# Optimization experiments

Measured on AMD Instinct MI355X. Metric: run time of the kernel, lower is better.

## Reference

```python
import jax, jax.numpy as jnp
import numpy as np

NHEAD = 8
GROUPS = 32   # GroupNorm(32) assumed for ConvNormActivation's norm (diffusion-UNet convention)
EPS = 1e-5


def group_norm(x, scale, bias):
    # x: [B, C, H, W]
    b, c, h, w = x.shape
    xg = x.reshape(b, GROUPS, c // GROUPS, h, w)
    mu = xg.mean(axis=(2, 3, 4), keepdims=True)
    var = xg.var(axis=(2, 3, 4), keepdims=True)
    xg = (xg - mu) * jax.lax.rsqrt(var + EPS)
    return xg.reshape(b, c, h, w) * scale[None, :, None, None] + bias[None, :, None, None]


def setup_inputs() -> dict:
    key = jax.random.key(0)
    ks = jax.random.split(key, 3)
    B, C, H, W = 8, 512, 32, 32
    s = 0.02
    return {
        "x": jax.random.normal(ks[0], (B, C, H, W), jnp.float32),
        "gn1_scale": jnp.ones((C,), jnp.float32),
        "gn1_bias": jnp.zeros((C,), jnp.float32),
        "w_qkv": jax.random.normal(ks[1], (3 * C, C), jnp.float32) * s,  # 1x1 conv kernel
        "b_qkv": jnp.zeros((3 * C,), jnp.float32),
        "w_proj": jax.random.normal(ks[2], (C, C), jnp.float32) * s,    # 1x1 conv kernel
        "b_proj": jnp.zeros((C,), jnp.float32),
        "gn2_scale": jnp.ones((C,), jnp.float32),
        "gn2_bias": jnp.zeros((C,), jnp.float32),
    }


def reference(x, gn1_scale, gn1_bias, w_qkv, b_qkv, w_proj, b_proj, gn2_scale, gn2_bias):
    b, c, h, w = x.shape
    n = h * w
    ch = c // NHEAD

    # qkv = Conv1x1(GroupNorm(x))  (norm_first=True)
    hn = group_norm(x, gn1_scale, gn1_bias)
    qkv = jnp.einsum('bchw,oc->bohw', hn, w_qkv) + b_qkv[None, :, None, None]

    # [B, 3C, H, W] -> [B*heads, 3*ch, N], split into q,k,v (matches torch reshape/split)
    qkv = qkv.reshape(b * NHEAD, 3 * ch, n)
    q, k, v = jnp.split(qkv, 3, axis=1)

    scale = ch ** -0.25
    wgt = jnp.einsum('bct,bcs->bts', q * scale, k * scale)   # [B*H, N, N]
    wgt = jax.nn.softmax(wgt, axis=-1)                        # stable (max-subtract fused)
    a = jnp.einsum('bts,bcs->bct', wgt, v).reshape(b, c, h, w)

    # proj_out = GroupNorm(Conv1x1(a))  (norm after conv, Identity activation)
    out = jnp.einsum('bchw,oc->bohw', a, w_proj) + b_proj[None, :, None, None]
    out = group_norm(out, gn2_scale, gn2_bias)
    return x + out
```

## Files before the change

kernel.cpp:

```cpp
#include <hip/hip_runtime.h>
#include <math.h>

#define NB 8
#define NC 512
#define NHW 1024
#define NG 32
#define CPG 16
#define QKV_C 1536
#define EPS 1e-5f
#define QSCALE 0.18033688011112042f

typedef float  f32x4  __attribute__((ext_vector_type(4)));
typedef __bf16 bf16x8 __attribute__((ext_vector_type(8)));
typedef __bf16 bf16x4 __attribute__((ext_vector_type(4)));
typedef short  s16x4  __attribute__((ext_vector_type(4)));

__device__ __forceinline__ void gload_lds16(const void* g, void* l) {
    __builtin_amdgcn_global_load_lds(
        (const __attribute__((address_space(1))) void*)g,
        (__attribute__((address_space(3))) void*)l, 16, 0, 0);
}

__device__ __forceinline__ void dma_drain() {
    asm volatile("s_waitcnt vmcnt(0)" ::: "memory");
}

__device__ __forceinline__ f32x4 mfma16(bf16x4 a, bf16x4 b, f32x4 c) {
#if __has_builtin(__builtin_amdgcn_mfma_f32_16x16x16bf16_1k)
    return __builtin_amdgcn_mfma_f32_16x16x16bf16_1k(
        __builtin_bit_cast(s16x4, a), __builtin_bit_cast(s16x4, b), c, 0, 0, 0);
#else
    f32x4 d;
    asm volatile("v_mfma_f32_16x16x16_bf16 %0, %1, %2, %3"
                 : "=v"(d) : "v"(a), "v"(b), "v"(c));
    return d;
#endif
}

__global__ __launch_bounds__(256) void prep_k(const float* __restrict__ x,
                                              float* __restrict__ mu,
                                              float* __restrict__ rinv,
                                              const float* __restrict__ w1,
                                              __bf16* __restrict__ d1,
                                              const float* __restrict__ w2,
                                              __bf16* __restrict__ d2,
                                              float* __restrict__ gstat) {
    const int bi = blockIdx.x;
    if (bi < 256) {
        const int grp = bi;
        const float4* p4 = (const float4*)(x + (size_t)grp * (CPG * NHW));
        float s = 0.f, s2 = 0.f;
        for (int i = threadIdx.x; i < CPG * NHW / 4; i += 256) {
            float4 v = p4[i];
            s  += v.x + v.y + v.z + v.w;
            s2 += v.x * v.x + v.y * v.y + v.z * v.z + v.w * v.w;
        }
        for (int off = 32; off > 0; off >>= 1) {
            s  += __shfl_down(s, off);
            s2 += __shfl_down(s2, off);
        }
        __shared__ float ls[4], ls2[4];
        const int wv = threadIdx.x >> 6;
        if ((threadIdx.x & 63) == 0) { ls[wv] = s; ls2[wv] = s2; }
        __syncthreads();
        if (threadIdx.x == 0) {
            float S = ls[0] + ls[1] + ls[2] + ls[3];
            float S2 = ls2[0] + ls2[1] + ls2[2] + ls2[3];
            const float inv = 1.f / (float)(CPG * NHW);
            float m = S * inv;
            float var = S2 * inv - m * m;
            mu[grp] = m;
            rinv[grp] = rsqrtf(var + EPS);
        }
        if (bi == 0 && threadIdx.x < 256) {
            gstat[threadIdx.x] = 0.f;
            gstat[threadIdx.x + 256] = 0.f;
        }
    } else {
        const int n1_4 = QKV_C * NC / 4;
        const int i = (bi - 256) * 256 + threadIdx.x;
        const float4* s = (i < n1_4) ? (const float4*)w1 + i
                                     : (const float4*)w2 + (i - n1_4);
        bf16x4* d = (i < n1_4) ? (bf16x4*)d1 + i : (bf16x4*)d2 + (i - n1_4);
        float4 v = *s;
        bf16x4 o;
        o[0] = (__bf16)v.x; o[1] = (__bf16)v.y; o[2] = (__bf16)v.z; o[3] = (__bf16)v.w;
        *d = o;
    }
}

__global__ __launch_bounds__(256) void gn_apply_t_k(const float* __restrict__ x,
                                                    const float* __restrict__ mu,
                                                    const float* __restrict__ rinv,
                                                    const float* __restrict__ sc,
                                                    const float* __restrict__ bi,
                                                    __bf16* __restrict__ hnT) {
    __shared__ float T[64][65];
    const int tid = threadIdx.x;
    const int nb = blockIdx.x * 64, cb = blockIdx.y * 64, b = blockIdx.z;
    const int col = (tid & 15) * 4;
    const int rb = tid >> 4;
    #pragma unroll
    for (int rr = 0; rr < 4; rr++) {
        int cl = rr * 16 + rb;
        int c = cb + cl;
        int grp = b * NG + (c >> 4);
        float a = sc[c] * rinv[grp];
        float d = bi[c] - mu[grp] * a;
        float4 v4 = *(const float4*)&x[((size_t)(b * NC + c)) * NHW + nb + col];
        T[cl][col + 0] = v4.x * a + d;
        T[cl][col + 1] = v4.y * a + d;
        T[cl][col + 2] = v4.z * a + d;
        T[cl][col + 3] = v4.w * a + d;
    }
    __syncthreads();
    const int nl = tid >> 2;
    const int c0 = (tid & 3) * 16;
    bf16x8 o0, o1;
    #pragma unroll
    for (int i = 0; i < 8; i++) o0[i] = (__bf16)T[c0 + i][nl];
    #pragma unroll
    for (int i = 0; i < 8; i++) o1[i] = (__bf16)T[c0 + 8 + i][nl];
    __bf16* dst = hnT + ((size_t)(b * NHW + nb + nl)) * NC + cb + c0;
    *(bf16x8*)dst = o0;
    *(bf16x8*)(dst + 8) = o1;
}

__device__ __forceinline__ void mm_stage(const __bf16* __restrict__ W,
                                         const __bf16* __restrict__ Bm,
                                         int K, int m0, int n0, int k0,
                                         __bf16* As, __bf16* Bs) {
    const int tid = threadIdx.x;
    const int w = tid >> 6, lane = tid & 63;
    const int lr = lane >> 2, lk = (lane & 3) * 8;
    #pragma unroll
    for (int i = 0; i < 2; i++) {
        int rb = (w * 2 + i) * 16;
        gload_lds16(W  + (size_t)(m0 + rb + lr) * K + k0 + lk, As + rb * 32);
        gload_lds16(Bm + (size_t)(n0 + rb + lr) * K + k0 + lk, Bs + rb * 32);
    }
}

__device__ __forceinline__ void mm_core(const __bf16* __restrict__ W,
                                        const __bf16* __restrict__ Bm,
                                        int K, int m0, int n0,
                                        __bf16* As, __bf16* Bs,
                                        f32x4 (&acc)[4][4]) {
    const int tid = threadIdx.x;
    const int w = tid >> 6, lane = tid & 63;
    const int l15 = lane & 15, quad = lane >> 4;
    const int wm = (w & 1) * 64, wn = (w >> 1) * 64;
    const int nk = K >> 5;
    mm_stage(W, Bm, K, m0, n0, 0, As, Bs);
    for (int it = 0; it < nk; it++) {
        const int cur = (it & 1) * 4096;
        dma_drain();
        __syncthreads();
        if (it + 1 < nk)
            mm_stage(W, Bm, K, m0, n0, (it + 1) * 32, As + (4096 - cur), Bs + (4096 - cur));
        bf16x8 af[4], bfv[4];
        #pragma unroll
        for (int mi = 0; mi < 4; mi++)
            af[mi] = *(const bf16x8*)(As + cur + (wm + mi * 16 + l15) * 32 + quad * 8);
        #pragma unroll
        for (int ni = 0; ni < 4; ni++)
            bfv[ni] = *(const bf16x8*)(Bs + cur + (wn + ni * 16 + l15) * 32 + quad * 8);
        #pragma unroll
        for (int mi = 0; mi < 4; mi++)
            #pragma unroll
            for (int ni = 0; ni < 4; ni++)
                acc[mi][ni] = __builtin_amdgcn_mfma_f32_16x16x32_bf16(
                    af[mi], bfv[ni], acc[mi][ni], 0, 0, 0);
    }
}

__global__ __launch_bounds__(256) void qkv_gemm_k(const __bf16* __restrict__ W,
                                                  const __bf16* __restrict__ hnT,
                                                  const float* __restrict__ bias,
                                                  __bf16* __restrict__ qT,
                                                  __bf16* __restrict__ kT,
                                                  __bf16* __restrict__ v) {
    __shared__ __bf16 As[2 * 128 * 32];
    __shared__ __bf16 Bs[2 * 128 * 32];
    const int m0 = blockIdx.x * 128, n0 = blockIdx.y * 128, b = blockIdx.z;
    f32x4 acc[4][4] = {};
    mm_core(W, hnT + (size_t)b * NHW * NC, NC, m0, n0, As, Bs, acc);
    const int tid = threadIdx.x;
    const int w = tid >> 6, lane = tid & 63;
    const int l15 = lane & 15, quad = lane >> 4;
    const int wm = (w & 1) * 64, wn = (w >> 1) * 64;
    #pragma unroll
    for (int mi = 0; mi < 4; mi++) {
        #pragma unroll
        for (int r = 0; r < 4; r++) {
            int m = m0 + wm + mi * 16 + quad * 4 + r;
            float bb = bias[m];
            int h = m / 192;
            int rr = m - h * 192;
            int bh = b * 8 + h;
            #pragma unroll
            for (int ni = 0; ni < 4; ni++) {
                int n = n0 + wn + ni * 16 + l15;
                float val = acc[mi][ni][r] + bb;
                if (rr < 64) {
                    qT[((size_t)bh << 16) + n * 64 + rr] = (__bf16)(val * QSCALE);
                } else if (rr < 128) {
                    kT[((size_t)bh << 16) + n * 64 + (rr - 64)] = (__bf16)val;
                } else {
                    v[((size_t)(bh * 64 + rr - 128)) * NHW + n] = (__bf16)val;
                }
            }
        }
    }
}

__global__ __launch_bounds__(256) void proj_gemm_k(const __bf16* __restrict__ W,
                                                   const __bf16* __restrict__ aT,
                                                   const float* __restrict__ bias,
                                                   __bf16* __restrict__ projb,
                                                   float* __restrict__ gstat) {
    __shared__ __bf16 As[2 * 128 * 32];
    __shared__ __bf16 Bs[2 * 128 * 32];
    const int m0 = blockIdx.x * 128, n0 = blockIdx.y * 128, b = blockIdx.z;
    f32x4 acc[4][4] = {};
    mm_core(W, aT + (size_t)b * NHW * NC, NC, m0, n0, As, Bs, acc);
    const int tid = threadIdx.x;
    const int w = tid >> 6, lane = tid & 63;
    const int l15 = lane & 15, quad = lane >> 4;
    const int wm = (w & 1) * 64, wn = (w >> 1) * 64;
    float bsum[4] = {}, bsq[4] = {};
    #pragma unroll
    for (int mi = 0; mi < 4; mi++) {
        #pragma unroll
        for (int r = 0; r < 4; r++) {
            int m = m0 + wm + mi * 16 + quad * 4 + r;
            float bb = bias[m];
            #pragma unroll
            for (int ni = 0; ni < 4; ni++) {
                int n = n0 + wn + ni * 16 + l15;
                float val = acc[mi][ni][r] + bb;
                projb[((size_t)(b * NC + m)) * NHW + n] = (__bf16)val;
                bsum[mi] += val;
                bsq[mi] += val * val;
            }
        }
    }
    #pragma unroll
    for (int mi = 0; mi < 4; mi++) {
        float s = bsum[mi], q = bsq[mi];
        #pragma unroll
        for (int off = 1; off < 64; off <<= 1) {
            s += __shfl_xor(s, off);
            q += __shfl_xor(q, off);
        }
        if (lane == 0) {
            int grp = b * NG + ((m0 + wm) >> 4) + mi;
            atomicAdd(&gstat[grp], s);
            atomicAdd(&gstat[256 + grp], q);
        }
    }
}

__global__ __launch_bounds__(256) void attn_k(const __bf16* __restrict__ qT,
                                              const __bf16* __restrict__ kT,
                                              const __bf16* __restrict__ vv,
                                              __bf16* __restrict__ aT) {
    __shared__ __bf16 Kt[2 * 4096];
    __shared__ __bf16 Vt[2 * 4096];
    const int tid = threadIdx.x;
    const int w = tid >> 6, lane = tid & 63;
    const int l15 = lane & 15, quad = lane >> 4;
    const int lr = lane >> 2, lk = (lane & 3) * 8;
    const int bh = blockIdx.x, t0 = blockIdx.y * 128;
    const __bf16* qb = qT + ((size_t)bh << 16);
    const __bf16* kb = kT + ((size_t)bh << 16);
    const __bf16* vb = vv + ((size_t)bh << 6) * NHW;
    const int xmask = l15 & 14;

    bf16x8 qfr[2][2];
    #pragma unroll
    for (int tb = 0; tb < 2; tb++)
        #pragma unroll
        for (int ch = 0; ch < 2; ch++)
            qfr[tb][ch] = *(const bf16x8*)(qb + (size_t)(t0 + w * 32 + tb * 16 + l15) * 64
                                           + ch * 32 + quad * 8);
    #pragma unroll
    for (int i = 0; i < 4; i++) {
        int inst = w * 4 + i;
        if (inst < 8) {
            int ch = inst >> 2, sb = (inst & 3) * 16;
            gload_lds16(kb + (size_t)(sb + lr) * 64 + ch * 32 + lk,
                        Kt + ch * 2048 + sb * 32);
        } else {
            int ip = inst - 8;
            int c = ip * 8 + (lane >> 3);
            int m2 = (lane & 7) * 2;
            gload_lds16(vb + (size_t)c * NHW + 4 * (m2 ^ (c & 14)),
                        Vt + ip * 512);
        }
    }
    float lp[2] = {0.f, 0.f};
    f32x4 Oacc[2][4] = {};

    for (int it = 0; it < 16; it++) {
        const int cur = (it & 1) * 4096;
        const int nxt = 4096 - cur;
        dma_drain();
        __syncthreads();
        if (it + 1 < 16) {
            const int s0 = (it + 1) * 64;
            #pragma unroll
            for (int i = 0; i < 4; i++) {
                int inst = w * 4 + i;
                if (inst < 8) {
                    int ch = inst >> 2, sb = (inst & 3) * 16;
                    gload_lds16(kb + (size_t)(s0 + sb + lr) * 64 + ch * 32 + lk,
                                Kt + nxt + ch * 2048 + sb * 32);
                } else {
                    int ip = inst - 8;
                    int c = ip * 8 + (lane >> 3);
                    int m2 = (lane & 7) * 2;
                    gload_lds16(vb + (size_t)c * NHW + s0 + 4 * (m2 ^ (c & 14)),
                                Vt + nxt + ip * 512);
                }
            }
        }
        f32x4 sacc[2][4] = {};
        #pragma unroll
        for (int ch = 0; ch < 2; ch++)
            #pragma unroll
            for (int j = 0; j < 4; j++) {
                bf16x8 kfr = *(const bf16x8*)(Kt + cur + ch * 2048
                                              + (j * 16 + l15) * 32 + quad * 8);
                sacc[0][j] = __builtin_amdgcn_mfma_f32_16x16x32_bf16(
                    kfr, qfr[0][ch], sacc[0][j], 0, 0, 0);
                sacc[1][j] = __builtin_amdgcn_mfma_f32_16x16x32_bf16(
                    kfr, qfr[1][ch], sacc[1][j], 0, 0, 0);
            }
        bf16x4 pf[2][4];
        #pragma unroll
        for (int tb = 0; tb < 2; tb++)
            #pragma unroll
            for (int j = 0; j < 4; j++) {
                bf16x4 pk;
                #pragma unroll
                for (int r = 0; r < 4; r++) {
                    float pv = __builtin_amdgcn_exp2f(sacc[tb][j][r]);
                    lp[tb] += pv;
                    pk[r] = (__bf16)pv;
                }
                pf[tb][j] = pk;
            }
        #pragma unroll
        for (int jt = 0; jt < 4; jt++) {
            const __bf16* vbase = Vt + cur + (((jt * 4 + quad) ^ xmask) << 2);
            #pragma unroll
            for (int ci = 0; ci < 4; ci++) {
                bf16x4 vfr = *(const bf16x4*)(vbase + (ci * 16 + l15) * 64);
                Oacc[0][ci] = mfma16(pf[0][jt], vfr, Oacc[0][ci]);
                Oacc[1][ci] = mfma16(pf[1][jt], vfr, Oacc[1][ci]);
            }
        }
    }
    const int b = bh >> 3, hh = bh & 7;
    #pragma unroll
    for (int tb = 0; tb < 2; tb++) {
        float s = lp[tb];
        s += __shfl_xor(s, 16);
        s += __shfl_xor(s, 32);
        #pragma unroll
        for (int r = 0; r < 4; r++) {
            float inv = 1.f / __shfl(s, quad * 4 + r);
            int t = t0 + w * 32 + tb * 16 + quad * 4 + r;
            size_t base = ((size_t)(b * NHW + t)) * NC + hh * 64;
            #pragma unroll
            for (int ci = 0; ci < 4; ci++)
                aT[base + ci * 16 + l15] = (__bf16)(Oacc[tb][ci][r] * inv);
        }
    }
}

__global__ __launch_bounds__(256) void final_k(const float* __restrict__ x,
                                               const __bf16* __restrict__ pb,
                                               const float* __restrict__ gstat,
                                               const float* __restrict__ sc,
                                               const float* __restrict__ bi,
                                               float* __restrict__ out) {
    const int i4 = blockIdx.x * 256 + threadIdx.x;
    const int c  = (i4 >> 8) & (NC - 1);
    const int b  = i4 >> 17;
    const int grp = b * NG + (c >> 4);
    const float inv = 1.f / (float)(CPG * NHW);
    const float m = gstat[grp] * inv;
    const float var = gstat[256 + grp] * inv - m * m;
    const float r = rsqrtf(var + EPS);
    const float a = sc[c] * r;
    const float d = bi[c] - m * a;
    float4 xv = ((const float4*)x)[i4];
    bf16x4 pv = ((const bf16x4*)pb)[i4];
    float4 o = make_float4(xv.x + (float)pv[0] * a + d, xv.y + (float)pv[1] * a + d,
                           xv.z + (float)pv[2] * a + d, xv.w + (float)pv[3] * a + d);
    ((float4*)out)[i4] = o;
}

extern "C" void kernel_launch(void* const* d_in, const int* in_sizes, int n_in,
                              void* d_out, int out_size, void* d_ws, size_t ws_size,
                              hipStream_t stream) {
    const float* x      = (const float*)d_in[0];
    const float* gn1_s  = (const float*)d_in[1];
    const float* gn1_b  = (const float*)d_in[2];
    const float* w_qkv  = (const float*)d_in[3];
    const float* b_qkv  = (const float*)d_in[4];
    const float* w_proj = (const float*)d_in[5];
    const float* b_proj = (const float*)d_in[6];
    const float* gn2_s  = (const float*)d_in[7];
    const float* gn2_b  = (const float*)d_in[8];
    float* out = (float*)d_out;

    char* p = (char*)d_ws;
    __bf16* hnT   = (__bf16*)p;           p += (size_t)8 * 1024 * 512 * 2;
    __bf16* qT    = (__bf16*)p;           p += (size_t)64 * 1024 * 64 * 2;
    __bf16* kT    = (__bf16*)p;           p += (size_t)64 * 1024 * 64 * 2;
    __bf16* vB    = (__bf16*)p;           p += (size_t)64 * 64 * 1024 * 2;
    __bf16* aT    = (__bf16*)p;           p += (size_t)8 * 1024 * 512 * 2;
    __bf16* projb = (__bf16*)p;           p += (size_t)8 * 512 * 1024 * 2;
    __bf16* wq    = (__bf16*)p;           p += (size_t)QKV_C * NC * 2;
    __bf16* wp    = (__bf16*)p;           p += (size_t)NC * NC * 2;
    float*  mu1   = (float*)p;            p += 256 * 4;
    float*  ri1   = (float*)p;            p += 256 * 4;
    float*  gstat = (float*)p;            p += 512 * 4;

    prep_k<<<1280, 256, 0, stream>>>(x, mu1, ri1, w_qkv, wq, w_proj, wp, gstat);
    gn_apply_t_k<<<dim3(16, 8, 8), 256, 0, stream>>>(x, mu1, ri1, gn1_s, gn1_b, hnT);

    qkv_gemm_k<<<dim3(12, 8, 8), 256, 0, stream>>>(wq, hnT, b_qkv, qT, kT, vB);

    attn_k<<<dim3(64, 8), 256, 0, stream>>>(qT, kT, vB, aT);

    proj_gemm_k<<<dim3(4, 8, 8), 256, 0, stream>>>(wp, aT, b_proj, projb, gstat);

    final_k<<<4096, 256, 0, stream>>>(x, projb, gstat, gn2_s, gn2_b, out);
}
```

Before: 181.4 us.

## Split attention keys across waves, halve proj tile, vectorize qkv epilogue stores

The attention kernel now processes 64 queries per block, with each wave handling a distinct 16-key slice. Partial outputs and row sums are reduced across waves through shared memory, and the result is written as 16-byte vectors. This doubles the grid to 1024 blocks for better occupancy. The projection GEMM uses 64-row tiles with its own inline loop, doubling its grid, and the QKV epilogue writes q/k as bf16x4 vectors with a vector bias load. The cost is a serialized four-phase cross-wave reduction through shared memory and more K/V reloads per query.

Result: slower. 187.1 us (+3.2%).

```diff
diff --git a/kernel.cpp b/kernel.cpp
--- a/kernel.cpp
+++ b/kernel.cpp
@@ -191,53 +191,95 @@
     const int wm = (w & 1) * 64, wn = (w >> 1) * 64;
     #pragma unroll
     for (int mi = 0; mi < 4; mi++) {
-        #pragma unroll
-        for (int r = 0; r < 4; r++) {
-            int m = m0 + wm + mi * 16 + quad * 4 + r;
-            float bb = bias[m];
-            int h = m / 192;
-            int rr = m - h * 192;
-            int bh = b * 8 + h;
-            #pragma unroll
-            for (int ni = 0; ni < 4; ni++) {
-                int n = n0 + wn + ni * 16 + l15;
-                float val = acc[mi][ni][r] + bb;
-                if (rr < 64) {
-                    qT[((size_t)bh << 16) + n * 64 + rr] = (__bf16)(val * QSCALE);
-                } else if (rr < 128) {
-                    kT[((size_t)bh << 16) + n * 64 + (rr - 64)] = (__bf16)val;
-                } else {
-                    v[((size_t)(bh * 64 + rr - 128)) * NHW + n] = (__bf16)val;
-                }
+        const int mbase = m0 + wm + mi * 16 + quad * 4;
+        const f32x4 bb4 = *(const f32x4*)&bias[mbase];
+        const int h = mbase / 192;
+        const int rr = mbase - h * 192;
+        const int bh = b * 8 + h;
+        #pragma unroll
+        for (int ni = 0; ni < 4; ni++) {
+            const int n = n0 + wn + ni * 16 + l15;
+            f32x4 a4 = acc[mi][ni];
+            if (rr < 64) {
+                bf16x4 o;
+                #pragma unroll
+                for (int r = 0; r < 4; r++) o[r] = (__bf16)((a4[r] + bb4[r]) * QSCALE);
+                *(bf16x4*)&qT[((size_t)bh << 16) + n * 64 + rr] = o;
+            } else if (rr < 128) {
+                bf16x4 o;
+                #pragma unroll
+                for (int r = 0; r < 4; r++) o[r] = (__bf16)(a4[r] + bb4[r]);
+                *(bf16x4*)&kT[((size_t)bh << 16) + n * 64 + (rr - 64)] = o;
+            } else {
+                #pragma unroll
+                for (int r = 0; r < 4; r++)
+                    v[((size_t)(bh * 64 + rr - 128 + r)) * NHW + n] = (__bf16)(a4[r] + bb4[r]);
             }
         }
     }
 }
 
 __global__ __launch_bounds__(256) void proj_gemm_k(const __bf16* __restrict__ W,
-                                                   const __bf16* __restrict__ aT,
+                                                   const __bf16* __restrict__ aTin,
                                                    const float* __restrict__ bias,
                                                    __bf16* __restrict__ projb,
                                                    float* __restrict__ gstat) {
-    __shared__ __bf16 As[2 * 128 * 32];
+    __shared__ __bf16 As[2 * 64 * 32];
     __shared__ __bf16 Bs[2 * 128 * 32];
-    const int m0 = blockIdx.x * 128, n0 = blockIdx.y * 128, b = blockIdx.z;
-    f32x4 acc[4][4] = {};
-    mm_core(W, aT + (size_t)b * NHW * NC, NC, m0, n0, As, Bs, acc);
+    const int m0 = blockIdx.x * 64, n0 = blockIdx.y * 128, b = blockIdx.z;
+    const __bf16* Bm = aTin + (size_t)b * NHW * NC;
     const int tid = threadIdx.x;
     const int w = tid >> 6, lane = tid & 63;
     const int l15 = lane & 15, quad = lane >> 4;
-    const int wm = (w & 1) * 64, wn = (w >> 1) * 64;
+    const int lr = lane >> 2, lk = (lane & 3) * 8;
+    f32x4 acc[4][2] = {};
+    {
+        gload_lds16(W + (size_t)(m0 + w * 16 + lr) * NC + lk, As + (w * 16) * 32);
+        #pragma unroll
+        for (int i = 0; i < 2; i++) {
+            int rb = w * 32 + i * 16;
+            gload_lds16(Bm + (size_t)(n0 + rb + lr) * NC + lk, Bs + rb * 32);
+        }
+    }
+    for (int it = 0; it < 16; it++) {
+        const int curA = (it & 1) * 2048, curB = (it & 1) * 4096;
+        dma_drain();
+        __syncthreads();
+        if (it + 1 < 16) {
+            const int k0 = (it + 1) * 32;
+            gload_lds16(W + (size_t)(m0 + w * 16 + lr) * NC + k0 + lk,
+                        As + (2048 - curA) + (w * 16) * 32);
+            #pragma unroll
+            for (int i = 0; i < 2; i++) {
+                int rb = w * 32 + i * 16;
+                gload_lds16(Bm + (size_t)(n0 + rb + lr) * NC + k0 + lk,
+                            Bs + (4096 - curB) + rb * 32);
+            }
+        }
+        bf16x8 af[4], bfv[2];
+        #pragma unroll
+        for (int mi = 0; mi < 4; mi++)
+            af[mi] = *(const bf16x8*)(As + curA + (mi * 16 + l15) * 32 + quad * 8);
+        #pragma unroll
+        for (int ni = 0; ni < 2; ni++)
+            bfv[ni] = *(const bf16x8*)(Bs + curB + (w * 32 + ni * 16 + l15) * 32 + quad * 8);
+        #pragma unroll
+        for (int mi = 0; mi < 4; mi++)
+            #pragma unroll
+            for (int ni = 0; ni < 2; ni++)
+                acc[mi][ni] = __builtin_amdgcn_mfma_f32_16x16x32_bf16(
+                    af[mi], bfv[ni], acc[mi][ni], 0, 0, 0);
+    }
     float bsum[4] = {}, bsq[4] = {};
     #pragma unroll
     for (int mi = 0; mi < 4; mi++) {
         #pragma unroll
         for (int r = 0; r < 4; r++) {
-            int m = m0 + wm + mi * 16 + quad * 4 + r;
+            int m = m0 + mi * 16 + quad * 4 + r;
             float bb = bias[m];
             #pragma unroll
-            for (int ni = 0; ni < 4; ni++) {
-                int n = n0 + wn + ni * 16 + l15;
+            for (int ni = 0; ni < 2; ni++) {
+                int n = n0 + w * 32 + ni * 16 + l15;
                 float val = acc[mi][ni][r] + bb;
                 projb[((size_t)(b * NC + m)) * NHW + n] = (__bf16)val;
                 bsum[mi] += val;
@@ -254,7 +296,7 @@
             q += __shfl_xor(q, off);
         }
         if (lane == 0) {
-            int grp = b * NG + ((m0 + wm) >> 4) + mi;
+            int grp = b * NG + (m0 >> 4) + mi;
             atomicAdd(&gstat[grp], s);
             atomicAdd(&gstat[256 + grp], q);
         }
@@ -265,24 +307,27 @@
                                               const __bf16* __restrict__ kT,
                                               const __bf16* __restrict__ vv,
                                               __bf16* __restrict__ aT) {
-    __shared__ __bf16 Kt[2 * 4096];
-    __shared__ __bf16 Vt[2 * 4096];
+    __shared__ __align__(16) char smem[32768];
+    __bf16* Kt = (__bf16*)smem;
+    __bf16* Vt = (__bf16*)(smem + 16384);
+    float*  Om = (float*)smem;
+    float*  Lr = (float*)(smem + 17408);
     const int tid = threadIdx.x;
     const int w = tid >> 6, lane = tid & 63;
     const int l15 = lane & 15, quad = lane >> 4;
     const int lr = lane >> 2, lk = (lane & 3) * 8;
-    const int bh = blockIdx.x, t0 = blockIdx.y * 128;
+    const int bh = blockIdx.x, t0 = blockIdx.y * 64;
     const __bf16* qb = qT + ((size_t)bh << 16);
     const __bf16* kb = kT + ((size_t)bh << 16);
     const __bf16* vb = vv + ((size_t)bh << 6) * NHW;
     const int xmask = l15 & 14;
 
-    bf16x8 qfr[2][2];
-    #pragma unroll
-    for (int tb = 0; tb < 2; tb++)
+    bf16x8 qfr[4][2];
+    #pragma unroll
+    for (int tb = 0; tb < 4; tb++)
         #pragma unroll
         for (int ch = 0; ch < 2; ch++)
-            qfr[tb][ch] = *(const bf16x8*)(qb + (size_t)(t0 + w * 32 + tb * 16 + l15) * 64
+            qfr[tb][ch] = *(const bf16x8*)(qb + (size_t)(t0 + tb * 16 + l15) * 64
                                            + ch * 32 + quad * 8);
     #pragma unroll
     for (int i = 0; i < 4; i++) {
@@ -299,8 +344,8 @@
                         Vt + ip * 512);
         }
     }
-    float lp[2] = {0.f, 0.f};
-    f32x4 Oacc[2][4] = {};
+    float lp[4] = {};
+    f32x4 Oacc[4][4] = {};
 
     for (int it = 0; it < 16; it++) {
         const int cur = (it & 1) * 4096;
@@ -325,59 +370,77 @@
                 }
             }
         }
-        f32x4 sacc[2][4] = {};
-        #pragma unroll
-        for (int ch = 0; ch < 2; ch++)
-            #pragma unroll
-            for (int j = 0; j < 4; j++) {
-                bf16x8 kfr = *(const bf16x8*)(Kt + cur + ch * 2048
-                                              + (j * 16 + l15) * 32 + quad * 8);
-                sacc[0][j] = __builtin_amdgcn_mfma_f32_16x16x32_bf16(
-                    kfr, qfr[0][ch], sacc[0][j], 0, 0, 0);
-                sacc[1][j] = __builtin_amdgcn_mfma_f32_16x16x32_bf16(
-                    kfr, qfr[1][ch], sacc[1][j], 0, 0, 0);
+        f32x4 sacc[4] = {};
+        #pragma unroll
+        for (int ch = 0; ch < 2; ch++) {
+            bf16x8 kfr = *(const bf16x8*)(Kt + cur + ch * 2048
+                                          + (w * 16 + l15) * 32 + quad * 8);
+            #pragma unroll
+            for (int tb = 0; tb < 4; tb++)
+                sacc[tb] = __builtin_amdgcn_mfma_f32_16x16x32_bf16(
+                    kfr, qfr[tb][ch], sacc[tb], 0, 0, 0);
+        }
+        bf16x4 pf[4];
+        #pragma unroll
+        for (int tb = 0; tb < 4; tb++) {
+            bf16x4 pk;
+            #pragma unroll
+            for (int r = 0; r < 4; r++) {
+                float pv = __builtin_amdgcn_exp2f(sacc[tb][r]);
+                lp[tb] += pv;
+                pk[r] = (__bf16)pv;
             }
-        bf16x4 pf[2][4];
-        #pragma unroll
-        for (int tb = 0; tb < 2; tb++)
-            #pragma unroll
-            for (int j = 0; j < 4; j++) {
-                bf16x4 pk;
-                #pragma unroll
-                for (int r = 0; r < 4; r++) {
-                    float pv = __builtin_amdgcn_exp2f(sacc[tb][j][r]);
-                    lp[tb] += pv;
-                    pk[r] = (__bf16)pv;
-                }
-                pf[tb][j] = pk;
-            }
-        #pragma unroll
-        for (int jt = 0; jt < 4; jt++) {
-            const __bf16* vbase = Vt + cur + (((jt * 4 + quad) ^ xmask) << 2);
-            #pragma unroll
-            for (int ci = 0; ci < 4; ci++) {
-                bf16x4 vfr = *(const bf16x4*)(vbase + (ci * 16 + l15) * 64);
-                Oacc[0][ci] = mfma16(pf[0][jt], vfr, Oacc[0][ci]);
-                Oacc[1][ci] = mfma16(pf[1][jt], vfr, Oacc[1][ci]);
-            }
-        }
-    }
-    const int b = bh >> 3, hh = bh & 7;
-    #pragma unroll
-    for (int tb = 0; tb < 2; tb++) {
+            pf[tb] = pk;
+        }
+        #pragma unroll
+        for (int ci = 0; ci < 4; ci++) {
+            bf16x4 vfr = *(const bf16x4*)(Vt + cur + (((w * 4 + quad) ^ xmask) << 2)
+                                          + (ci * 16 + l15) * 64);
+            #pragma unroll
+            for (int tb = 0; tb < 4; tb++)
+                Oacc[tb][ci] = mfma16(pf[tb], vfr, Oacc[tb][ci]);
+        }
+    }
+    float lsum[4];
+    #pragma unroll
+    for (int tb = 0; tb < 4; tb++) {
         float s = lp[tb];
         s += __shfl_xor(s, 16);
         s += __shfl_xor(s, 32);
-        #pragma unroll
-        for (int r = 0; r < 4; r++) {
-            float inv = 1.f / __shfl(s, quad * 4 + r);
-            int t = t0 + w * 32 + tb * 16 + quad * 4 + r;
-            size_t base = ((size_t)(b * NHW + t)) * NC + hh * 64;
-            #pragma unroll
-            for (int ci = 0; ci < 4; ci++)
-                aT[base + ci * 16 + l15] = (__bf16)(Oacc[tb][ci][r] * inv);
-        }
-    }
+        lsum[tb] = s;
+    }
+    __syncthreads();
+    #pragma unroll
+    for (int ph = 0; ph < 4; ph++) {
+        if (w == ph) {
+            #pragma unroll
+            for (int tb = 0; tb < 4; tb++) {
+                #pragma unroll
+                for (int ci = 0; ci < 4; ci++) {
+                    float* dst = Om + (ci * 16 + l15) * 68 + tb * 16 + quad * 4;
+                    f32x4 val = Oacc[tb][ci];
+                    if (ph) val += *(const f32x4*)dst;
+                    *(f32x4*)dst = val;
+                }
+                if (quad == 0) {
+                    float* lt = Lr + tb * 16 + l15;
+                    *lt = (ph ? *lt : 0.f) + lsum[tb];
+                }
+            }
+        }
+        __syncthreads();
+    }
+    const int b = bh >> 3, hh = bh & 7;
+    const int t = tid >> 2, cb2 = (tid & 3) * 16;
+    const float linv = 1.f / Lr[t];
+    bf16x8 o0, o1;
+    #pragma unroll
+    for (int i = 0; i < 8; i++) o0[i] = (__bf16)(Om[(cb2 + i) * 68 + t] * linv);
+    #pragma unroll
+    for (int i = 0; i < 8; i++) o1[i] = (__bf16)(Om[(cb2 + 8 + i) * 68 + t] * linv);
+    __bf16* dst = aT + ((size_t)(b * NHW + t0 + t)) * NC + hh * 64 + cb2;
+    *(bf16x8*)dst = o0;
+    *(bf16x8*)(dst + 8) = o1;
 }
 
 __global__ __launch_bounds__(256) void final_k(const float* __restrict__ x,
@@ -435,9 +498,9 @@
 
     qkv_gemm_k<<<dim3(12, 8, 8), 256, 0, stream>>>(wq, hnT, b_qkv, qT, kT, vB);
 
-    attn_k<<<dim3(64, 8), 256, 0, stream>>>(qT, kT, vB, aT);
-
-    proj_gemm_k<<<dim3(4, 8, 8), 256, 0, stream>>>(wp, aT, b_proj, projb, gstat);
+    attn_k<<<dim3(64, 16), 256, 0, stream>>>(qT, kT, vB, aT);
+
+    proj_gemm_k<<<dim3(8, 8, 8), 256, 0, stream>>>(wp, aT, b_proj, projb, gstat);
 
     final_k<<<4096, 256, 0, stream>>>(x, projb, gstat, gn2_s, gn2_b, out);
 }
```
